# Kernel optimization log

Hardware: AMD Instinct MI355X
Metric: run time of the kernel (lower is better)

Reference implementation:

```python
import jax, jax.numpy as jnp
import numpy as np

N_OBJ, N_REL = 16384, 32768
HID, POOL = 512, 4096
N_OBJ_CLS, N_REL_CLS = 151, 51


def setup_inputs() -> dict:
    key = jax.random.key(0)
    ks = jax.random.split(key, 12)
    return {
        "edge_ctx": jax.random.normal(ks[0], (N_OBJ, HID), jnp.float32),
        "union_features": jax.random.normal(ks[1], (N_REL, POOL), jnp.float32),
        "pair_idx": jax.random.randint(ks[2], (N_REL, 2), 0, N_OBJ, jnp.int64) if jax.config.jax_enable_x64 else jax.random.randint(ks[2], (N_REL, 2), 0, N_OBJ, jnp.int32),
        "obj_preds": jax.random.randint(ks[3], (N_OBJ,), 0, N_OBJ_CLS, jnp.int32),
        "W_post_emb": jax.random.normal(ks[4], (2 * HID, HID), jnp.float32) * (10.0 / np.sqrt(HID)),
        "b_post_emb": jax.random.normal(ks[5], (2 * HID,), jnp.float32) * 0.01,
        "W_post_cat": jax.random.normal(ks[6], (POOL, 2 * HID), jnp.float32) * (1.0 / np.sqrt(2 * HID)),
        "b_post_cat": jax.random.normal(ks[7], (POOL,), jnp.float32) * 0.01,
        "W_rel": jax.random.normal(ks[8], (N_REL_CLS, POOL), jnp.float32) * (1.0 / np.sqrt(POOL)),
        "b_rel": jax.random.normal(ks[9], (N_REL_CLS,), jnp.float32) * 0.01,
        "freq_bias": jax.random.normal(ks[10], (N_OBJ_CLS, N_OBJ_CLS, N_REL_CLS), jnp.float32),
    }


def reference(edge_ctx, union_features, pair_idx, obj_preds,
              W_post_emb, b_post_emb, W_post_cat, b_post_cat,
              W_rel, b_rel, freq_bias):
    # post_emb: [N_obj, H] -> [N_obj, 2H] -> head/tail reps [N_obj, H]
    edge_rep = edge_ctx @ W_post_emb.T + b_post_emb            # [N_obj, 2H]
    edge_rep = edge_rep.reshape(edge_rep.shape[0], 2, HID)
    head_rep = edge_rep[:, 0]                                  # [N_obj, H]
    tail_rep = edge_rep[:, 1]                                  # [N_obj, H]

    h_idx = pair_idx[:, 0]
    t_idx = pair_idx[:, 1]
    # gather + concat head/tail pair features -> [N_rel, 2H]
    prod_rep = jnp.concatenate([head_rep[h_idx], tail_rep[t_idx]], axis=-1)
    # post_cat linear -> [N_rel, POOL]
    prod_rep = prod_rep @ W_post_cat.T + b_post_cat
    # use_vision, pooling_dim == MLP_HEAD_DIM -> elementwise product
    prod_rep = prod_rep * union_features
    # rel_compress -> [N_rel, num_rel_cls]
    rel_dists = prod_rep @ W_rel.T + b_rel
    # frequency bias lookup indexed by (head class, tail class)
    bias = freq_bias[obj_preds[h_idx], obj_preds[t_idx]]       # [N_rel, num_rel_cls]
    return rel_dists + bias
```

## Files before the change

### kernel.cpp

```cpp
#include <hip/hip_runtime.h>

#define N_OBJ 16384
#define N_REL 32768
#define HID 512
#define POOL 4096
#define NCLS 151
#define NRELCLS 51

#define AS1 __attribute__((address_space(1)))
#define AS3 __attribute__((address_space(3)))

typedef __attribute__((ext_vector_type(8))) short short8;
typedef __attribute__((ext_vector_type(4))) float f32x4;

__device__ __forceinline__ unsigned short f2bf(float x) {
    unsigned u = __float_as_uint(x);
    u += 0x7fff + ((u >> 16) & 1);
    return (unsigned short)(u >> 16);
}

__global__ void cvt_kernel(const float* __restrict__ in, unsigned short* __restrict__ out, long n8) {
    long i = (long)blockIdx.x * blockDim.x + threadIdx.x;
    if (i >= n8) return;
    const float4* p = (const float4*)in;
    float4 a = p[2 * i], b = p[2 * i + 1];
    short8 o;
    o[0] = f2bf(a.x); o[1] = f2bf(a.y); o[2] = f2bf(a.z); o[3] = f2bf(a.w);
    o[4] = f2bf(b.x); o[5] = f2bf(b.y); o[6] = f2bf(b.z); o[7] = f2bf(b.w);
    ((short8*)out)[i] = o;
}

__global__ void cvt_wrel_kernel(const float* __restrict__ W, unsigned short* __restrict__ out) {
    int gid = blockIdx.x * 256 + threadIdx.x;
    int row = gid >> 9;
    int c8 = (gid & 511) << 3;
    short8 o = {};
    if (row < NRELCLS) {
        const float* src = W + (long)row * POOL + c8;
        float4 a = *(const float4*)src, b = *(const float4*)(src + 4);
        o[0] = f2bf(a.x); o[1] = f2bf(a.y); o[2] = f2bf(a.z); o[3] = f2bf(a.w);
        o[4] = f2bf(b.x); o[5] = f2bf(b.y); o[6] = f2bf(b.z); o[7] = f2bf(b.w);
    }
    *(short8*)(out + (long)row * POOL + c8) = o;
}

__device__ __forceinline__ void stage_tile128x64(const unsigned short* __restrict__ src,
                                                 unsigned short* lds,
                                                 int row0, int rowStrideElems, int col0,
                                                 int wave, int lane) {
    const char* s = (const char*)(src + (long)row0 * rowStrideElems + col0);
    long strideB = (long)rowStrideElems * 2;
#pragma unroll
    for (int is = 0; is < 4; ++is) {
        int issue = wave * 4 + is;
        const char* g = s + (long)(issue * 8 + (lane >> 3)) * strideB + (lane & 7) * 16;
        __builtin_amdgcn_global_load_lds((const AS1 void*)g,
                                         (AS3 void*)((char*)lds + issue * 1024),
                                         16, 0, 0);
    }
}

__global__ __launch_bounds__(256) void gemm1_kernel(const unsigned short* __restrict__ A,
                                                    const unsigned short* __restrict__ B,
                                                    const float* __restrict__ bias,
                                                    unsigned short* __restrict__ C) {
    __shared__ __align__(16) unsigned short At[128 * 64];
    __shared__ __align__(16) unsigned short Bt[128 * 64];
    int row0 = blockIdx.x * 128, col0 = blockIdx.y * 128;
    int tid = threadIdx.x, wave = tid >> 6, lane = tid & 63;
    int wr = (wave >> 1) * 64, wc = (wave & 1) * 64;
    int lrow = lane & 15, lko = (lane >> 4) * 8;
    f32x4 acc[4][4] = {};
    for (int kt = 0; kt < HID / 64; ++kt) {
        stage_tile128x64(A, At, row0, HID, kt * 64, wave, lane);
        stage_tile128x64(B, Bt, col0, HID, kt * 64, wave, lane);
        __syncthreads();
#pragma unroll
        for (int ks = 0; ks < 2; ++ks) {
            short8 af[4], bf[4];
#pragma unroll
            for (int mi = 0; mi < 4; ++mi) af[mi] = *(const short8*)(At + (wr + 16 * mi + lrow) * 64 + ks * 32 + lko);
#pragma unroll
            for (int ni = 0; ni < 4; ++ni) bf[ni] = *(const short8*)(Bt + (wc + 16 * ni + lrow) * 64 + ks * 32 + lko);
#pragma unroll
            for (int mi = 0; mi < 4; ++mi)
#pragma unroll
                for (int ni = 0; ni < 4; ++ni)
                    acc[mi][ni] = __builtin_amdgcn_mfma_f32_16x16x32_bf16(af[mi], bf[ni], acc[mi][ni], 0, 0, 0);
        }
        __syncthreads();
    }
#pragma unroll
    for (int mi = 0; mi < 4; ++mi)
#pragma unroll
        for (int ni = 0; ni < 4; ++ni)
#pragma unroll
            for (int i = 0; i < 4; ++i) {
                int r = row0 + wr + 16 * mi + 4 * (lane >> 4) + i;
                int c = col0 + wc + 16 * ni + lrow;
                C[(long)r * 1024 + c] = f2bf(acc[mi][ni][i] + bias[c]);
            }
}

__global__ void gather_kernel(const unsigned short* __restrict__ edge_rep,
                              const int* __restrict__ pair_idx,
                              unsigned short* __restrict__ A2) {
    long gid = (long)blockIdx.x * 256 + threadIdx.x;
    int r = (int)(gid >> 7), j = (int)(gid & 127);
    int src = (j < 64) ? pair_idx[2 * r] : pair_idx[2 * r + 1];
    const uint4* s = (const uint4*)(edge_rep + (long)src * 1024);
    ((uint4*)(A2 + (long)r * 1024))[j] = s[j];
}

__global__ void init_out_kernel(const int* __restrict__ pair_idx, const int* __restrict__ obj_preds,
                                const float* __restrict__ b_rel, const float* __restrict__ freq_bias,
                                float* __restrict__ out) {
    int r = blockIdx.x * 4 + (threadIdx.x >> 6);
    int lane = threadIdx.x & 63;
    if (lane < NRELCLS) {
        int h = pair_idx[2 * r], t = pair_idx[2 * r + 1];
        long idx = ((long)obj_preds[h] * NCLS + obj_preds[t]) * NRELCLS + lane;
        out[(long)r * NRELCLS + lane] = b_rel[lane] + freq_bias[idx];
    }
}

__device__ __forceinline__ void stage_ab(const char* __restrict__ A2b, const char* __restrict__ Wcb,
                                         char* lds, int slot, int t, int row0, int col0,
                                         int w, int lane) {
    int kb = t * 64;
#pragma unroll
    for (int i = 0; i < 2; ++i) {
        int obase = i * 8192 + w * 1024;
        int o = obase + lane * 16;
        int row = o >> 6, cin = o & 63;
        int c = cin ^ ((row & 3) << 4);
        __builtin_amdgcn_global_load_lds((const AS1 void*)(A2b + (long)(row0 + row) * 2048 + kb + c),
                                         (AS3 void*)(lds + slot + obase), 16, 0, 0);
        __builtin_amdgcn_global_load_lds((const AS1 void*)(Wcb + (long)(col0 + row) * 2048 + kb + c),
                                         (AS3 void*)(lds + 49152 + slot + obase), 16, 0, 0);
    }
}

__device__ __forceinline__ void kstep(const char* lds, int slot, int wr, int wc, int lrow, int lcb,
                                      f32x4 acc[8][4]) {
    const char* A = lds + slot;
    const char* B = lds + 49152 + slot;
    short8 bfr[4];
#pragma unroll
    for (int ni = 0; ni < 4; ++ni) {
        int r = wc + 16 * ni + lrow;
        bfr[ni] = *(const short8*)(B + r * 64 + (lcb ^ ((r & 3) << 4)));
    }
    __builtin_amdgcn_s_setprio(1);
#pragma unroll
    for (int mi = 0; mi < 8; ++mi) {
        int r = wr + 16 * mi + lrow;
        short8 a = *(const short8*)(A + r * 64 + (lcb ^ ((r & 3) << 4)));
#pragma unroll
        for (int ni = 0; ni < 4; ++ni)
            acc[mi][ni] = __builtin_amdgcn_mfma_f32_16x16x32_bf16(a, bfr[ni], acc[mi][ni], 0, 0, 0);
    }
    __builtin_amdgcn_s_setprio(0);
}

__global__ __launch_bounds__(512, 2) void fused_kernel(
    const unsigned short* __restrict__ A2,
    const unsigned short* __restrict__ Wcat,
    const unsigned short* __restrict__ Wrelp,
    const float* __restrict__ unionf,
    const float* __restrict__ bcat,
    float* __restrict__ out) {
    __shared__ __align__(16) char lds[98304];
    int row0 = blockIdx.x * 256, col0 = blockIdx.y * 256;
    int tid = threadIdx.x, w = tid >> 6, lane = tid & 63;
    int wr = (w >> 2) * 128, wc = (w & 3) * 64;
    int lrow = lane & 15, lcb = (lane >> 4) * 16;
    const char* A2b = (const char*)A2;
    const char* Wcb = (const char*)Wcat;
    f32x4 acc2[8][4] = {};

    stage_ab(A2b, Wcb, lds, 0, 0, row0, col0, w, lane);
    stage_ab(A2b, Wcb, lds, 16384, 1, row0, col0, w, lane);

    int slot = 0, stslot = 32768;
    for (int t = 0; t < 31; ++t) {
        asm volatile("s_waitcnt vmcnt(4)" ::: "memory");
        __builtin_amdgcn_s_barrier();
        __builtin_amdgcn_sched_barrier(0);
        if (t < 30) stage_ab(A2b, Wcb, lds, stslot, t + 2, row0, col0, w, lane);
        kstep(lds, slot, wr, wc, lrow, lcb, acc2);
        slot = (slot == 32768) ? 0 : slot + 16384;
        stslot = (stslot == 32768) ? 0 : stslot + 16384;
    }
    asm volatile("s_waitcnt vmcnt(0)" ::: "memory");
    __builtin_amdgcn_s_barrier();
    __builtin_amdgcn_sched_barrier(0);
    kstep(lds, slot, wr, wc, lrow, lcb, acc2);

    asm volatile("s_waitcnt lgkmcnt(0)" ::: "memory");
    __builtin_amdgcn_sched_barrier(0);
    __builtin_amdgcn_s_barrier();
    __builtin_amdgcn_sched_barrier(0);

#pragma unroll
    for (int h = 0; h < 2; ++h)
#pragma unroll
        for (int i = 0; i < 2; ++i) {
            int obase = i * 8192 + w * 1024;
            int o = obase + lane * 16;
            int rw = o >> 8, cin = o & 255;
            int c = cin ^ ((rw & 7) << 4);
            __builtin_amdgcn_global_load_lds(
                (const AS1 void*)((const char*)Wrelp + (long)rw * 8192 + (col0 + h * 128) * 2 + c),
                (AS3 void*)(lds + 65536 + h * 16384 + obase), 16, 0, 0);
        }

    f32x4 acc3[2][4] = {};
#pragma unroll
    for (int h = 0; h < 2; ++h) {
        if (((w & 3) >> 1) == h) {
            int pc0 = ((w & 3) & 1) * 64;
            float bcv[4];
#pragma unroll
            for (int ni = 0; ni < 4; ++ni) bcv[ni] = bcat[col0 + h * 128 + pc0 + 16 * ni + lrow];
#pragma unroll
            for (int mi = 0; mi < 8; ++mi)
#pragma unroll
                for (int ni = 0; ni < 4; ++ni) {
                    int pcol = pc0 + 16 * ni + lrow;
#pragma unroll
                    for (int i = 0; i < 4; ++i) {
                        int prow = wr + 16 * mi + 4 * (lane >> 4) + i;
                        float u = unionf[(long)(row0 + prow) * 4096 + col0 + h * 128 + pcol];
                        *(unsigned short*)(lds + prow * 256 + ((pcol * 2) ^ ((prow & 7) << 4)))
                            = f2bf((acc2[mi][ni][i] + bcv[ni]) * u);
                    }
                }
        }
        asm volatile("s_waitcnt vmcnt(0) lgkmcnt(0)" ::: "memory");
        __builtin_amdgcn_sched_barrier(0);
        __builtin_amdgcn_s_barrier();
        __builtin_amdgcn_sched_barrier(0);
#pragma unroll
        for (int ks = 0; ks < 4; ++ks) {
            int cb2 = ks * 64 + lcb;
            short8 wb[4], pa[2];
#pragma unroll
            for (int ni = 0; ni < 4; ++ni) {
                int r = 16 * ni + lrow;
                wb[ni] = *(const short8*)(lds + 65536 + h * 16384 + r * 256 + (cb2 ^ ((r & 7) << 4)));
            }
#pragma unroll
            for (int mi = 0; mi < 2; ++mi) {
                int r = w * 32 + 16 * mi + lrow;
                pa[mi] = *(const short8*)(lds + r * 256 + (cb2 ^ ((r & 7) << 4)));
            }
#pragma unroll
            for (int mi = 0; mi < 2; ++mi)
#pragma unroll
                for (int ni = 0; ni < 4; ++ni)
                    acc3[mi][ni] = __builtin_amdgcn_mfma_f32_16x16x32_bf16(pa[mi], wb[ni], acc3[mi][ni], 0, 0, 0);
        }
        if (h == 0) {
            __builtin_amdgcn_s_barrier();
            __builtin_amdgcn_sched_barrier(0);
        }
    }
#pragma unroll
    for (int mi = 0; mi < 2; ++mi)
#pragma unroll
        for (int ni = 0; ni < 4; ++ni)
#pragma unroll
            for (int i = 0; i < 4; ++i) {
                int r = row0 + w * 32 + 16 * mi + 4 * (lane >> 4) + i;
                int cc = 16 * ni + lrow;
                if (cc < NRELCLS) atomicAdd(out + (long)r * NRELCLS + cc, acc3[mi][ni][i]);
            }
}

extern "C" void kernel_launch(void* const* d_in, const int* in_sizes, int n_in,
                              void* d_out, int out_size, void* d_ws, size_t ws_size,
                              hipStream_t stream) {
    const float* edge_ctx  = (const float*)d_in[0];
    const float* unionf    = (const float*)d_in[1];
    const int*   pair_idx  = (const int*)d_in[2];
    const int*   obj_preds = (const int*)d_in[3];
    const float* W_emb     = (const float*)d_in[4];
    const float* b_emb     = (const float*)d_in[5];
    const float* W_cat     = (const float*)d_in[6];
    const float* b_cat     = (const float*)d_in[7];
    const float* W_rel     = (const float*)d_in[8];
    const float* b_rel     = (const float*)d_in[9];
    const float* freq_bias = (const float*)d_in[10];
    float* out = (float*)d_out;

    char* ws = (char*)d_ws;
    unsigned short* ecb   = (unsigned short*)ws; ws += (size_t)N_OBJ * HID * 2;
    unsigned short* Wembb = (unsigned short*)ws; ws += (size_t)1024 * HID * 2;
    unsigned short* Wcatb = (unsigned short*)ws; ws += (size_t)POOL * 1024 * 2;
    unsigned short* Wrelb = (unsigned short*)ws; ws += (size_t)64 * POOL * 2;
    unsigned short* erep  = (unsigned short*)ws; ws += (size_t)N_OBJ * 1024 * 2;
    unsigned short* A2    = (unsigned short*)ws; ws += (size_t)N_REL * 1024 * 2;

    cvt_kernel<<<4096, 256, 0, stream>>>(edge_ctx, ecb, (long)N_OBJ * HID / 8);
    cvt_kernel<<<256, 256, 0, stream>>>(W_emb, Wembb, (long)1024 * HID / 8);
    cvt_kernel<<<2048, 256, 0, stream>>>(W_cat, Wcatb, (long)POOL * 1024 / 8);
    cvt_wrel_kernel<<<128, 256, 0, stream>>>(W_rel, Wrelb);
    gemm1_kernel<<<dim3(128, 8), 256, 0, stream>>>(ecb, Wembb, b_emb, erep);
    gather_kernel<<<16384, 256, 0, stream>>>(erep, pair_idx, A2);
    init_out_kernel<<<8192, 256, 0, stream>>>(pair_idx, obj_preds, b_rel, freq_bias, out);
    fused_kernel<<<dim3(128, 16), 512, 0, stream>>>(A2, Wcatb, Wrelb, unionf, b_cat, out);
}
```

Before: 565.0 us.

## Halve fused GEMM column tile, triple-buffer K loop, stage union features via LDS

Shrinks the fused kernel's output tile from 256x256 to 256x128 and doubles the grid. The K loop becomes a three-stage LDS ring. The union-feature epilogue now stages coalesced tiles into LDS with async global-to-LDS loads instead of strided per-element global reads, and the W_rel slice is prefetched at kernel start. This aims to cut epilogue load latency and improve pipelining. The cost is reloading A from global twice as often, doubling the atomic adds, and an LDS footprint near the per-CU limit that likely allows only one block per CU.

```diff
diff --git a/kernel.cpp b/kernel.cpp
--- a/kernel.cpp
+++ b/kernel.cpp
@@ -9,6 +9,12 @@
 
 #define AS1 __attribute__((address_space(1)))
 #define AS3 __attribute__((address_space(3)))
+
+#define ABASE 0
+#define BBASE 49152
+#define PBOFF 73728
+#define WROFF 139264
+#define LDSSZ 155648
 
 typedef __attribute__((ext_vector_type(8))) short short8;
 typedef __attribute__((ext_vector_type(4))) float f32x4;
@@ -125,7 +131,7 @@
 }
 
 __device__ __forceinline__ void stage_ab(const char* __restrict__ A2b, const char* __restrict__ Wcb,
-                                         char* lds, int slot, int t, int row0, int col0,
+                                         char* lds, int s, int t, int row0, int col0,
                                          int w, int lane) {
     int kb = t * 64;
 #pragma unroll
@@ -135,16 +141,22 @@
         int row = o >> 6, cin = o & 63;
         int c = cin ^ ((row & 3) << 4);
         __builtin_amdgcn_global_load_lds((const AS1 void*)(A2b + (long)(row0 + row) * 2048 + kb + c),
-                                         (AS3 void*)(lds + slot + obase), 16, 0, 0);
+                                         (AS3 void*)(lds + ABASE + s * 16384 + obase), 16, 0, 0);
+    }
+    {
+        int obase = w * 1024;
+        int o = obase + lane * 16;
+        int row = o >> 6, cin = o & 63;
+        int c = cin ^ ((row & 3) << 4);
         __builtin_amdgcn_global_load_lds((const AS1 void*)(Wcb + (long)(col0 + row) * 2048 + kb + c),
-                                         (AS3 void*)(lds + 49152 + slot + obase), 16, 0, 0);
-    }
-}
-
-__device__ __forceinline__ void kstep(const char* lds, int slot, int wr, int wc, int lrow, int lcb,
-                                      f32x4 acc[8][4]) {
-    const char* A = lds + slot;
-    const char* B = lds + 49152 + slot;
+                                         (AS3 void*)(lds + BBASE + s * 8192 + obase), 16, 0, 0);
+    }
+}
+
+__device__ __forceinline__ void kstep(const char* lds, int s, int wr, int wc, int lrow, int lcb,
+                                      f32x4 acc[4][4]) {
+    const char* A = lds + ABASE + s * 16384;
+    const char* B = lds + BBASE + s * 8192;
     short8 bfr[4];
 #pragma unroll
     for (int ni = 0; ni < 4; ++ni) {
@@ -153,7 +165,7 @@
     }
     __builtin_amdgcn_s_setprio(1);
 #pragma unroll
-    for (int mi = 0; mi < 8; ++mi) {
+    for (int mi = 0; mi < 4; ++mi) {
         int r = wr + 16 * mi + lrow;
         short8 a = *(const short8*)(A + r * 64 + (lcb ^ ((r & 3) << 4)));
 #pragma unroll
@@ -161,6 +173,19 @@
             acc[mi][ni] = __builtin_amdgcn_mfma_f32_16x16x32_bf16(a, bfr[ni], acc[mi][ni], 0, 0, 0);
     }
     __builtin_amdgcn_s_setprio(0);
+}
+
+__device__ __forceinline__ void stage_u(const char* __restrict__ ub, char* lds, int buf, int c,
+                                        int row0, int col0, int w, int lane) {
+#pragma unroll
+    for (int i = 0; i < 2; ++i) {
+        int obase = i * 8192 + w * 1024;
+        int o = obase + lane * 16;
+        int row = o >> 6, cin = o & 63;
+        __builtin_amdgcn_global_load_lds(
+            (const AS1 void*)(ub + (long)(row0 + row) * 16384 + (long)(col0 + 16 * c) * 4 + cin),
+            (AS3 void*)(lds + buf * 16384 + obase), 16, 0, 0);
+    }
 }
 
 __global__ __launch_bounds__(512, 2) void fused_kernel(
@@ -170,101 +195,95 @@
     const float* __restrict__ unionf,
     const float* __restrict__ bcat,
     float* __restrict__ out) {
-    __shared__ __align__(16) char lds[98304];
-    int row0 = blockIdx.x * 256, col0 = blockIdx.y * 256;
+    __shared__ __align__(16) char lds[LDSSZ];
+    int row0 = blockIdx.x * 256, col0 = blockIdx.y * 128;
     int tid = threadIdx.x, w = tid >> 6, lane = tid & 63;
-    int wr = (w >> 2) * 128, wc = (w & 3) * 64;
+    int wr = (w >> 1) * 64, wc = (w & 1) * 64;
     int lrow = lane & 15, lcb = (lane >> 4) * 16;
     const char* A2b = (const char*)A2;
     const char* Wcb = (const char*)Wcat;
-    f32x4 acc2[8][4] = {};
-
+    f32x4 acc2[4][4] = {};
+
+#pragma unroll
+    for (int i = 0; i < 2; ++i) {
+        int obase = i * 8192 + w * 1024;
+        int o = obase + lane * 16;
+        int rw = o >> 8, cin = o & 255;
+        int c = cin ^ ((rw & 7) << 4);
+        __builtin_amdgcn_global_load_lds(
+            (const AS1 void*)((const char*)Wrelp + (long)rw * 8192 + col0 * 2 + c),
+            (AS3 void*)(lds + WROFF + obase), 16, 0, 0);
+    }
     stage_ab(A2b, Wcb, lds, 0, 0, row0, col0, w, lane);
-    stage_ab(A2b, Wcb, lds, 16384, 1, row0, col0, w, lane);
-
-    int slot = 0, stslot = 32768;
+    stage_ab(A2b, Wcb, lds, 1, 1, row0, col0, w, lane);
+
     for (int t = 0; t < 31; ++t) {
-        asm volatile("s_waitcnt vmcnt(4)" ::: "memory");
+        asm volatile("s_waitcnt vmcnt(3)" ::: "memory");
         __builtin_amdgcn_s_barrier();
         __builtin_amdgcn_sched_barrier(0);
-        if (t < 30) stage_ab(A2b, Wcb, lds, stslot, t + 2, row0, col0, w, lane);
-        kstep(lds, slot, wr, wc, lrow, lcb, acc2);
-        slot = (slot == 32768) ? 0 : slot + 16384;
-        stslot = (stslot == 32768) ? 0 : stslot + 16384;
+        if (t < 30) stage_ab(A2b, Wcb, lds, (t + 2) % 3, t + 2, row0, col0, w, lane);
+        kstep(lds, t % 3, wr, wc, lrow, lcb, acc2);
     }
     asm volatile("s_waitcnt vmcnt(0)" ::: "memory");
     __builtin_amdgcn_s_barrier();
     __builtin_amdgcn_sched_barrier(0);
-    kstep(lds, slot, wr, wc, lrow, lcb, acc2);
-
-    asm volatile("s_waitcnt lgkmcnt(0)" ::: "memory");
-    __builtin_amdgcn_sched_barrier(0);
+    kstep(lds, 31 % 3, wr, wc, lrow, lcb, acc2);
     __builtin_amdgcn_s_barrier();
     __builtin_amdgcn_sched_barrier(0);
 
-#pragma unroll
-    for (int h = 0; h < 2; ++h)
-#pragma unroll
-        for (int i = 0; i < 2; ++i) {
-            int obase = i * 8192 + w * 1024;
-            int o = obase + lane * 16;
-            int rw = o >> 8, cin = o & 255;
-            int c = cin ^ ((rw & 7) << 4);
-            __builtin_amdgcn_global_load_lds(
-                (const AS1 void*)((const char*)Wrelp + (long)rw * 8192 + (col0 + h * 128) * 2 + c),
-                (AS3 void*)(lds + 65536 + h * 16384 + obase), 16, 0, 0);
-        }
-
-    f32x4 acc3[2][4] = {};
-#pragma unroll
-    for (int h = 0; h < 2; ++h) {
-        if (((w & 3) >> 1) == h) {
-            int pc0 = ((w & 3) & 1) * 64;
-            float bcv[4];
-#pragma unroll
-            for (int ni = 0; ni < 4; ++ni) bcv[ni] = bcat[col0 + h * 128 + pc0 + 16 * ni + lrow];
-#pragma unroll
-            for (int mi = 0; mi < 8; ++mi)
-#pragma unroll
-                for (int ni = 0; ni < 4; ++ni) {
-                    int pcol = pc0 + 16 * ni + lrow;
-#pragma unroll
-                    for (int i = 0; i < 4; ++i) {
-                        int prow = wr + 16 * mi + 4 * (lane >> 4) + i;
-                        float u = unionf[(long)(row0 + prow) * 4096 + col0 + h * 128 + pcol];
-                        *(unsigned short*)(lds + prow * 256 + ((pcol * 2) ^ ((prow & 7) << 4)))
-                            = f2bf((acc2[mi][ni][i] + bcv[ni]) * u);
-                    }
-                }
-        }
-        asm volatile("s_waitcnt vmcnt(0) lgkmcnt(0)" ::: "memory");
+    const char* ub = (const char*)unionf;
+    stage_u(ub, lds, 0, 0, row0, col0, w, lane);
+    stage_u(ub, lds, 1, 4, row0, col0, w, lane);
+    stage_u(ub, lds, 2, 1, row0, col0, w, lane);
+    stage_u(ub, lds, 3, 5, row0, col0, w, lane);
+#pragma unroll
+    for (int r = 0; r < 4; ++r) {
+        if (r < 3) { asm volatile("s_waitcnt vmcnt(4)" ::: "memory"); }
+        else       { asm volatile("s_waitcnt vmcnt(0)" ::: "memory"); }
+        __builtin_amdgcn_s_barrier();
+        __builtin_amdgcn_sched_barrier(0);
+        int buf = 2 * (r & 1) + (w & 1);
+        int colp0 = (w & 1) * 64 + 16 * r;
+        float bcv = bcat[col0 + colp0 + lrow];
+        const char* U = lds + buf * 16384;
+#pragma unroll
+        for (int mi = 0; mi < 4; ++mi)
+#pragma unroll
+            for (int i = 0; i < 4; ++i) {
+                int prow = wr + 16 * mi + 4 * (lane >> 4) + i;
+                float u = *(const float*)(U + prow * 64 + lrow * 4);
+                float v = (acc2[mi][r][i] + bcv) * u;
+                int colp = colp0 + lrow;
+                *(unsigned short*)(lds + PBOFF + prow * 256 + ((colp * 2) ^ ((prow & 7) << 4))) = f2bf(v);
+            }
+        asm volatile("s_waitcnt lgkmcnt(0)" ::: "memory");
         __builtin_amdgcn_sched_barrier(0);
         __builtin_amdgcn_s_barrier();
         __builtin_amdgcn_sched_barrier(0);
-#pragma unroll
-        for (int ks = 0; ks < 4; ++ks) {
-            int cb2 = ks * 64 + lcb;
-            short8 wb[4], pa[2];
-#pragma unroll
-            for (int ni = 0; ni < 4; ++ni) {
-                int r = 16 * ni + lrow;
-                wb[ni] = *(const short8*)(lds + 65536 + h * 16384 + r * 256 + (cb2 ^ ((r & 7) << 4)));
-            }
-#pragma unroll
-            for (int mi = 0; mi < 2; ++mi) {
-                int r = w * 32 + 16 * mi + lrow;
-                pa[mi] = *(const short8*)(lds + r * 256 + (cb2 ^ ((r & 7) << 4)));
-            }
-#pragma unroll
-            for (int mi = 0; mi < 2; ++mi)
-#pragma unroll
-                for (int ni = 0; ni < 4; ++ni)
-                    acc3[mi][ni] = __builtin_amdgcn_mfma_f32_16x16x32_bf16(pa[mi], wb[ni], acc3[mi][ni], 0, 0, 0);
+        if (r == 0) { stage_u(ub, lds, 0, 2, row0, col0, w, lane); stage_u(ub, lds, 1, 6, row0, col0, w, lane); }
+        if (r == 1) { stage_u(ub, lds, 2, 3, row0, col0, w, lane); stage_u(ub, lds, 3, 7, row0, col0, w, lane); }
+    }
+
+    f32x4 acc3[2][4] = {};
+#pragma unroll
+    for (int ks = 0; ks < 4; ++ks) {
+        int cb2 = ks * 64 + lcb;
+        short8 wb[4], pa[2];
+#pragma unroll
+        for (int ni = 0; ni < 4; ++ni) {
+            int r2 = 16 * ni + lrow;
+            wb[ni] = *(const short8*)(lds + WROFF + r2 * 256 + (cb2 ^ ((r2 & 7) << 4)));
         }
-        if (h == 0) {
-            __builtin_amdgcn_s_barrier();
-            __builtin_amdgcn_sched_barrier(0);
+#pragma unroll
+        for (int mi = 0; mi < 2; ++mi) {
+            int r2 = w * 32 + 16 * mi + lrow;
+            pa[mi] = *(const short8*)(lds + PBOFF + r2 * 256 + (cb2 ^ ((r2 & 7) << 4)));
         }
+#pragma unroll
+        for (int mi = 0; mi < 2; ++mi)
+#pragma unroll
+            for (int ni = 0; ni < 4; ++ni)
+                acc3[mi][ni] = __builtin_amdgcn_mfma_f32_16x16x32_bf16(pa[mi], wb[ni], acc3[mi][ni], 0, 0, 0);
     }
 #pragma unroll
     for (int mi = 0; mi < 2; ++mi)
@@ -309,5 +328,5 @@
     gemm1_kernel<<<dim3(128, 8), 256, 0, stream>>>(ecb, Wembb, b_emb, erep);
     gather_kernel<<<16384, 256, 0, stream>>>(erep, pair_idx, A2);
     init_out_kernel<<<8192, 256, 0, stream>>>(pair_idx, obj_preds, b_rel, freq_bias, out);
-    fused_kernel<<<dim3(128, 16), 512, 0, stream>>>(A2, Wcatb, Wrelb, unionf, b_cat, out);
-}
+    fused_kernel<<<dim3(128, 32), 512, 0, stream>>>(A2, Wcatb, Wrelb, unionf, b_cat, out);
+}
```

New measurement: 749.3 us. +32.6%, slower.
